# Performance work log

Measured on AMD Instinct MI355X. Metric: run time of the kernel, lower is better.

The kernel has to match this reference:

```python
import jax, jax.numpy as jnp
import numpy as np

B, D, H, E, K = 4096, 1024, 4096, 8, 2

def setup_inputs() -> dict:
    key = jax.random.key(0)
    ks = jax.random.split(key, 6)
    return {
        "x_modality": jax.random.normal(ks[0], (B, D), dtype=jnp.float32),
        "expert_indices": jax.random.randint(ks[1], (B, K), 0, E, dtype=jnp.int32),
        "hard_weights": jax.random.uniform(ks[2], (B, K), dtype=jnp.float32),
        "w1": jax.random.normal(ks[3], (E, D, H), dtype=jnp.float32) * (1.0 / np.sqrt(D)),
        "b1": jnp.zeros((E, H), dtype=jnp.float32),
        "w2": jax.random.normal(ks[4], (E, H, D), dtype=jnp.float32) * (1.0 / np.sqrt(H)),
        "b2": jnp.zeros((E, D), dtype=jnp.float32),
    }

def reference(x_modality, expert_indices, hard_weights, w1, b1, w2, b2):
    b = x_modality.shape[0]
    # Per-token gate per expert: sum of hard_weights over top_k slots routed to that expert.
    gates = jnp.zeros((b, E), dtype=x_modality.dtype)
    gates = gates.at[jnp.arange(b)[:, None], expert_indices].add(hard_weights)  # [b, E]
    # Dense expert compute (small fixed E), then gated combine.
    h = jax.nn.gelu(jnp.einsum("bd,edh->ebh", x_modality, w1) + b1[:, None, :], approximate=False)
    y = jnp.einsum("ebh,ehd->ebd", h, w2) + b2[:, None, :]  # [E, b, D]
    return jnp.einsum("be,ebd->bd", gates, y)
```

## Files before the change

kernel.cpp:

```cpp
#include <hip/hip_runtime.h>
#include <hip/hip_bf16.h>
#include <math.h>

#define NB 4096
#define ND 1024
#define NH 4096
#define NE 8
#define NKK 2
#define NROWS (NB*NKK)
#define MAXT 72

typedef __attribute__((ext_vector_type(8))) short short8;
typedef __attribute__((ext_vector_type(4))) float f32x4;

__device__ __forceinline__ void gload_lds16(const void* g, void* l) {
    __builtin_amdgcn_global_load_lds(
        (const __attribute__((address_space(1))) unsigned int*)g,
        (__attribute__((address_space(3))) unsigned int*)l, 16, 0, 0);
}

__device__ __forceinline__ unsigned short f2bf(float f) {
    __hip_bfloat16 h = __float2bfloat16(f);
    return *reinterpret_cast<unsigned short*>(&h);
}

__device__ __forceinline__ float fast_gelu(float x) {
    float xs  = x * 0.70710678118654752f;
    float axs = fabsf(xs);
    float t   = __builtin_amdgcn_rcpf(1.0f + 0.3275911f * axs);
    float p   = t * (0.254829592f + t * (-0.284496736f + t * (1.421413741f +
                t * (-1.453152027f + t * 1.061405429f))));
    float e   = __expf(-xs * xs);
    float erf_abs = 1.0f - p * e;
    float erf = copysignf(erf_abs, x);
    return 0.5f * x * (1.0f + erf);
}


__global__ void k_cvt_x(const float* __restrict__ in, __hip_bfloat16* __restrict__ out, int n8) {
    int i = blockIdx.x * 256 + threadIdx.x;
    if (i >= n8) return;
    const float4* p = reinterpret_cast<const float4*>(in) + (size_t)i * 2;
    float4 a = p[0], b = p[1];
    ushort4 lo, hi;
    lo.x = f2bf(a.x); lo.y = f2bf(a.y); lo.z = f2bf(a.z); lo.w = f2bf(a.w);
    hi.x = f2bf(b.x); hi.y = f2bf(b.y); hi.z = f2bf(b.z); hi.w = f2bf(b.w);
    reinterpret_cast<ushort4*>(out)[(size_t)i*2]   = lo;
    reinterpret_cast<ushort4*>(out)[(size_t)i*2+1] = hi;
}

__global__ void k_transpose_cvt(const float* __restrict__ in, __hip_bfloat16* __restrict__ out,
                                int R, int C) {
    __shared__ float tile[64][68];
    const size_t ebase = (size_t)blockIdx.z * R * C;
    const int r0 = blockIdx.y * 64, c0 = blockIdx.x * 64;
    const int t = threadIdx.x;
    const int lr = t >> 4, lc4 = (t & 15) * 4;
    #pragma unroll
    for (int i = 0; i < 4; ++i) {
        int r = lr + i * 16;
        float4 v = *reinterpret_cast<const float4*>(&in[ebase + (size_t)(r0 + r) * C + (c0 + lc4)]);
        *reinterpret_cast<float4*>(&tile[r][lc4]) = v;
    }
    __syncthreads();
    const int q = t & 15, cw = t >> 4;
    #pragma unroll
    for (int i = 0; i < 4; ++i) {
        int cc = cw + i * 16;
        ushort4 v;
        v.x = f2bf(tile[q*4+0][cc]);
        v.y = f2bf(tile[q*4+1][cc]);
        v.z = f2bf(tile[q*4+2][cc]);
        v.w = f2bf(tile[q*4+3][cc]);
        *reinterpret_cast<ushort4*>(&out[ebase + (size_t)(c0 + cc) * R + (r0 + q*4)]) = v;
    }
}


__global__ void k_route_count(const int* __restrict__ idx, int* cnt) {
    int b = blockIdx.x * 256 + threadIdx.x;
    if (b < NB) {
        atomicAdd(&cnt[idx[2*b]], 1);
        atomicAdd(&cnt[idx[2*b+1]], 1);
    }
}

__global__ void k_route_scan(const int* __restrict__ cnt, int* offs, int* cursor,
                             int* tile_e, int* tile_row, int* ntiles) {
    if (threadIdx.x == 0) {
        int s = 0, t = 0;
        for (int e = 0; e < NE; ++e) {
            offs[e] = s; cursor[e] = s;
            for (int r = 0; r < cnt[e]; r += 128) {
                tile_e[t] = e; tile_row[t] = s + r; ++t;
            }
            s += cnt[e];
        }
        offs[NE] = s;
        *ntiles = t;
    }
}

__global__ void k_route_fill(const int* __restrict__ idx, const float* __restrict__ hw,
                             int* cursor, int* tok, float* gw) {
    int b = blockIdx.x * 256 + threadIdx.x;
    if (b < NB) {
        #pragma unroll
        for (int k = 0; k < NKK; ++k) {
            int e = idx[2*b + k];
            int p = atomicAdd(&cursor[e], 1);
            tok[p] = b;
            gw[p]  = hw[2*b + k];
        }
    }
}


template<int STAGE>
__global__ __launch_bounds__(256, 4) void moe_gemm(
    const __hip_bfloat16* __restrict__ Asrc,
    const __hip_bfloat16* __restrict__ Bt,
    const float* __restrict__ bias,
    __hip_bfloat16* __restrict__ Hout,
    float* __restrict__ Out,
    const int* __restrict__ offs,
    const int* __restrict__ tok,
    const float* __restrict__ gw,
    const int* __restrict__ tile_e,
    const int* __restrict__ tile_row,
    const int* __restrict__ ntiles)
{
    constexpr int N = (STAGE == 1) ? NH : ND;
    constexpr int K = (STAGE == 1) ? ND : NH;
    constexpr int NT_N = N / 128;
    constexpr int NTL = NT_N / 8;
    constexpr int TOTAL = NT_N * MAXT;

    const int bid = blockIdx.x;
    const int xcd = bid & 7;
    const int c = bid >> 3;
    const int tb  = c / (NTL * 9);
    const int rr  = c % (NTL * 9);
    const int ntl = rr / 9;
    const int tin = rr % 9;
    const int tile = tb * 9 + tin;
    const int nt = xcd * NTL + ntl;
    if (tile >= *ntiles) return;

    const int e = tile_e[tile];
    const int rowbase = tile_row[tile];
    const int end = offs[e + 1];

    __shared__ __align__(16) __hip_bfloat16 sA[128 * 64];
    __shared__ __align__(16) __hip_bfloat16 sB[128 * 64];

    const int tid = threadIdx.x;
    const int w = tid >> 6;
    const int l = tid & 63;

    const int srow = tid >> 3;
    const int schunk = (tid & 7) ^ (srow & 7);
    const __hip_bfloat16* aptr[4];
    const __hip_bfloat16* bptr[4];
    #pragma unroll
    for (int i = 0; i < 4; ++i) {
        int r = srow + i * 32;
        int re = rowbase + r; if (re > end - 1) re = end - 1;
        if (STAGE == 1) aptr[i] = Asrc + (size_t)tok[re] * ND + schunk * 8;
        else            aptr[i] = Asrc + (size_t)re * NH + schunk * 8;
        bptr[i] = Bt + ((size_t)e * N + (nt * 128 + r)) * K + schunk * 8;
    }
    __hip_bfloat16 *adst[4], *bdst[4];
    #pragma unroll
    for (int i = 0; i < 4; ++i) {
        adst[i] = sA + (i * 256 + w * 64) * 8;
        bdst[i] = sB + (i * 256 + w * 64) * 8;
    }

    const int wm = (w >> 1) * 64;
    const int wn = (w & 1) * 64;
    const int l15 = l & 15, l4 = l >> 4;

    f32x4 acc[4][4];
    #pragma unroll
    for (int mi = 0; mi < 4; ++mi)
        #pragma unroll
        for (int ni = 0; ni < 4; ++ni) acc[mi][ni] = (f32x4){0.f, 0.f, 0.f, 0.f};

    int aoff[4][2], boff[4][2];
    #pragma unroll
    for (int mi = 0; mi < 4; ++mi) {
        int row = wm + mi * 16 + l15;
        #pragma unroll
        for (int ks = 0; ks < 2; ++ks)
            aoff[mi][ks] = row * 128 + (((ks * 4 + l4) ^ (row & 7)) * 16);
    }
    #pragma unroll
    for (int ni = 0; ni < 4; ++ni) {
        int row = wn + ni * 16 + l15;
        #pragma unroll
        for (int ks = 0; ks < 2; ++ks)
            boff[ni][ks] = row * 128 + (((ks * 4 + l4) ^ (row & 7)) * 16);
    }

    const char* sAb = (const char*)sA;
    const char* sBb = (const char*)sB;

    for (int kt = 0; kt < K / 64; ++kt) {
        #pragma unroll
        for (int i = 0; i < 4; ++i) {
            gload_lds16(aptr[i] + kt * 64, adst[i]);
            gload_lds16(bptr[i] + kt * 64, bdst[i]);
        }
        __syncthreads();
        short8 af[4][2], bfr[4][2];
        #pragma unroll
        for (int mi = 0; mi < 4; ++mi)
            #pragma unroll
            for (int ks = 0; ks < 2; ++ks)
                af[mi][ks] = *(const short8*)(sAb + aoff[mi][ks]);
        #pragma unroll
        for (int ni = 0; ni < 4; ++ni)
            #pragma unroll
            for (int ks = 0; ks < 2; ++ks)
                bfr[ni][ks] = *(const short8*)(sBb + boff[ni][ks]);
        #pragma unroll
        for (int mi = 0; mi < 4; ++mi)
            #pragma unroll
            for (int ni = 0; ni < 4; ++ni)
                #pragma unroll
                for (int ks = 0; ks < 2; ++ks)
                    acc[mi][ni] = __builtin_amdgcn_mfma_f32_16x16x32_bf16(
                        af[mi][ks], bfr[ni][ks], acc[mi][ni], 0, 0, 0);
        __syncthreads();
    }

    const int ncol0 = nt * 128 + wn;
    #pragma unroll
    for (int mi = 0; mi < 4; ++mi) {
        #pragma unroll
        for (int ni = 0; ni < 4; ++ni) {
            int gn = ncol0 + ni * 16 + l15;
            float bv = bias[e * N + gn];
            #pragma unroll
            for (int j = 0; j < 4; ++j) {
                int re = rowbase + wm + mi * 16 + l4 * 4 + j;
                if (re < end) {
                    float v = acc[mi][ni][j] + bv;
                    if (STAGE == 1) {
                        Hout[(size_t)re * NH + gn] = __float2bfloat16(fast_gelu(v));
                    } else {
                        atomicAdd(&Out[(size_t)tok[re] * ND + gn], gw[re] * v);
                    }
                }
            }
        }
    }
}


extern "C" void kernel_launch(void* const* d_in, const int* in_sizes, int n_in,
                              void* d_out, int out_size, void* d_ws, size_t ws_size,
                              hipStream_t stream) {
    const float* x   = (const float*)d_in[0];
    const int*   idx = (const int*)d_in[1];
    const float* hw  = (const float*)d_in[2];
    const float* w1  = (const float*)d_in[3];
    const float* b1  = (const float*)d_in[4];
    const float* w2  = (const float*)d_in[5];
    const float* b2  = (const float*)d_in[6];
    float* out = (float*)d_out;

    char* ws = (char*)d_ws;
    size_t off = 0;
    __hip_bfloat16* xb  = (__hip_bfloat16*)(ws + off); off += (size_t)NB * ND * 2;
    __hip_bfloat16* w1t = (__hip_bfloat16*)(ws + off); off += (size_t)NE * ND * NH * 2;
    __hip_bfloat16* w2t = (__hip_bfloat16*)(ws + off); off += (size_t)NE * NH * ND * 2;
    __hip_bfloat16* h   = (__hip_bfloat16*)(ws + off); off += (size_t)NROWS * NH * 2;
    int*   tok     = (int*)(ws + off);   off += NROWS * 4;
    float* gwb     = (float*)(ws + off); off += NROWS * 4;
    int*   cnt     = (int*)(ws + off);   off += 16 * 4;
    int*   offs    = (int*)(ws + off);   off += 16 * 4;
    int*   cursor  = (int*)(ws + off);   off += 16 * 4;
    int*   tile_e  = (int*)(ws + off);   off += MAXT * 4;
    int*   tile_row= (int*)(ws + off);   off += MAXT * 4;
    int*   ntiles  = (int*)(ws + off);   off += 16 * 4;
    (void)ws_size; (void)in_sizes; (void)n_in; (void)out_size;

    hipMemsetAsync(d_out, 0, (size_t)NB * ND * sizeof(float), stream);
    hipMemsetAsync(cnt, 0, 16 * 4, stream);

    k_cvt_x<<<dim3((NB * ND / 8 + 255) / 256), 256, 0, stream>>>(x, xb, NB * ND / 8);
    k_transpose_cvt<<<dim3(NH / 64, ND / 64, NE), 256, 0, stream>>>(w1, w1t, ND, NH);
    k_transpose_cvt<<<dim3(ND / 64, NH / 64, NE), 256, 0, stream>>>(w2, w2t, NH, ND);
    k_route_count<<<dim3((NB + 255) / 256), 256, 0, stream>>>(idx, cnt);
    k_route_scan<<<1, 64, 0, stream>>>(cnt, offs, cursor, tile_e, tile_row, ntiles);
    k_route_fill<<<dim3((NB + 255) / 256), 256, 0, stream>>>(idx, hw, cursor, tok, gwb);

    moe_gemm<1><<<dim3((NH / 128) * MAXT), 256, 0, stream>>>(
        xb, w1t, b1, h, nullptr, offs, tok, gwb, tile_e, tile_row, ntiles);
    moe_gemm<2><<<dim3((ND / 128) * MAXT), 256, 0, stream>>>(
        h, w2t, b2, nullptr, out, offs, tok, gwb, tile_e, tile_row, ntiles);
}
```

Measured before the change: 404.5 us.

## Enlarge MoE GEMM tiles to 256 rows, double-buffer LDS, split-K second stage

Routing tiles grow from 128 to 256 rows. Both grouped GEMMs now run with 512 threads, larger block tiles (256x256 in stage 1, 256x128 in stage 2) and double-buffered LDS staging through dynamic shared memory, with MFMA sections raised to higher wave priority. The x conversion becomes a gather into expert-sorted row order, so stage 1 reads A contiguously. Stage 2 splits K into two halves across XCD pairs, which doubles the atomic adds into the output. The aim is more data reuse per block and loads that overlap compute, at the cost of lower occupancy and more atomic traffic.

```diff
diff --git a/kernel.cpp b/kernel.cpp
--- a/kernel.cpp
+++ b/kernel.cpp
@@ -8,7 +8,7 @@
 #define NE 8
 #define NKK 2
 #define NROWS (NB*NKK)
-#define MAXT 72
+#define MAXT2 40
 
 typedef __attribute__((ext_vector_type(8))) short short8;
 typedef __attribute__((ext_vector_type(4))) float f32x4;
@@ -37,18 +37,6 @@
 }
 
 
-__global__ void k_cvt_x(const float* __restrict__ in, __hip_bfloat16* __restrict__ out, int n8) {
-    int i = blockIdx.x * 256 + threadIdx.x;
-    if (i >= n8) return;
-    const float4* p = reinterpret_cast<const float4*>(in) + (size_t)i * 2;
-    float4 a = p[0], b = p[1];
-    ushort4 lo, hi;
-    lo.x = f2bf(a.x); lo.y = f2bf(a.y); lo.z = f2bf(a.z); lo.w = f2bf(a.w);
-    hi.x = f2bf(b.x); hi.y = f2bf(b.y); hi.z = f2bf(b.z); hi.w = f2bf(b.w);
-    reinterpret_cast<ushort4*>(out)[(size_t)i*2]   = lo;
-    reinterpret_cast<ushort4*>(out)[(size_t)i*2+1] = hi;
-}
-
 __global__ void k_transpose_cvt(const float* __restrict__ in, __hip_bfloat16* __restrict__ out,
                                 int R, int C) {
     __shared__ float tile[64][68];
@@ -91,7 +79,7 @@
         int s = 0, t = 0;
         for (int e = 0; e < NE; ++e) {
             offs[e] = s; cursor[e] = s;
-            for (int r = 0; r < cnt[e]; r += 128) {
+            for (int r = 0; r < cnt[e]; r += 256) {
                 tile_e[t] = e; tile_row[t] = s + r; ++t;
             }
             s += cnt[e];
@@ -115,9 +103,17 @@
     }
 }
 
+__global__ void k_gather_cvt(const float* __restrict__ x, const int* __restrict__ tok,
+                             __hip_bfloat16* __restrict__ Ag) {
+    const int row = blockIdx.x;
+    const float4 v = reinterpret_cast<const float4*>(x + (size_t)tok[row] * ND)[threadIdx.x];
+    ushort4 u; u.x = f2bf(v.x); u.y = f2bf(v.y); u.z = f2bf(v.z); u.w = f2bf(v.w);
+    reinterpret_cast<ushort4*>(Ag + (size_t)row * ND)[threadIdx.x] = u;
+}
+
 
 template<int STAGE>
-__global__ __launch_bounds__(256, 4) void moe_gemm(
+__global__ __launch_bounds__(512, 2) void moe_gemm(
     const __hip_bfloat16* __restrict__ Asrc,
     const __hip_bfloat16* __restrict__ Bt,
     const float* __restrict__ bias,
@@ -130,126 +126,119 @@
     const int* __restrict__ tile_row,
     const int* __restrict__ ntiles)
 {
-    constexpr int N = (STAGE == 1) ? NH : ND;
-    constexpr int K = (STAGE == 1) ? ND : NH;
-    constexpr int NT_N = N / 128;
-    constexpr int NTL = NT_N / 8;
-    constexpr int TOTAL = NT_N * MAXT;
+    constexpr int N   = (STAGE == 1) ? NH : ND;
+    constexpr int K   = (STAGE == 1) ? ND : NH;
+    constexpr int BN  = (STAGE == 1) ? 256 : 128;
+    constexpr int KT  = (STAGE == 1) ? 16 : 32;
+    constexpr int NI  = BN / 64;
+    constexpr int BR  = (BN * 64) / (512 * 8);
+    constexpr int ASZ = 256 * 64;
+    constexpr int BUF = ASZ + BN * 64;
+
+    extern __shared__ __hip_bfloat16 smem[];
 
     const int bid = blockIdx.x;
     const int xcd = bid & 7;
-    const int c = bid >> 3;
-    const int tb  = c / (NTL * 9);
-    const int rr  = c % (NTL * 9);
-    const int ntl = rr / 9;
-    const int tin = rr % 9;
-    const int tile = tb * 9 + tin;
-    const int nt = xcd * NTL + ntl;
+    const int c   = bid >> 3;
+    const int tile = (xcd >> 1) * 10 + (c >> 3);
+    const int sub  = c & 7;
     if (tile >= *ntiles) return;
+
+    int nt, kbase;
+    if (STAGE == 1) { nt = (xcd & 1) * 8 + sub; kbase = 0; }
+    else            { nt = sub;                 kbase = (xcd & 1) * (NH / 2); }
 
     const int e = tile_e[tile];
     const int rowbase = tile_row[tile];
     const int end = offs[e + 1];
 
-    __shared__ __align__(16) __hip_bfloat16 sA[128 * 64];
-    __shared__ __align__(16) __hip_bfloat16 sB[128 * 64];
-
     const int tid = threadIdx.x;
-    const int w = tid >> 6;
-    const int l = tid & 63;
-
+    const int w = tid >> 6, l = tid & 63;
     const int srow = tid >> 3;
     const int schunk = (tid & 7) ^ (srow & 7);
+
     const __hip_bfloat16* aptr[4];
-    const __hip_bfloat16* bptr[4];
-    #pragma unroll
-    for (int i = 0; i < 4; ++i) {
-        int r = srow + i * 32;
-        int re = rowbase + r; if (re > end - 1) re = end - 1;
-        if (STAGE == 1) aptr[i] = Asrc + (size_t)tok[re] * ND + schunk * 8;
-        else            aptr[i] = Asrc + (size_t)re * NH + schunk * 8;
-        bptr[i] = Bt + ((size_t)e * N + (nt * 128 + r)) * K + schunk * 8;
-    }
-    __hip_bfloat16 *adst[4], *bdst[4];
-    #pragma unroll
-    for (int i = 0; i < 4; ++i) {
-        adst[i] = sA + (i * 256 + w * 64) * 8;
-        bdst[i] = sB + (i * 256 + w * 64) * 8;
-    }
-
-    const int wm = (w >> 1) * 64;
-    const int wn = (w & 1) * 64;
+    #pragma unroll
+    for (int r = 0; r < 4; ++r) {
+        int re = rowbase + srow + r * 64; if (re > end - 1) re = end - 1;
+        aptr[r] = Asrc + (size_t)re * K + kbase + schunk * 8;
+    }
+    const __hip_bfloat16* bptr[BR];
+    #pragma unroll
+    for (int r = 0; r < BR; ++r)
+        bptr[r] = Bt + ((size_t)e * N + (size_t)(nt * BN + srow + r * 64)) * K + kbase + schunk * 8;
+
+    const int wm  = (w >> 2) * 128;
+    const int wn  = (w & 3) * (BN / 4);
     const int l15 = l & 15, l4 = l >> 4;
 
-    f32x4 acc[4][4];
-    #pragma unroll
-    for (int mi = 0; mi < 4; ++mi)
-        #pragma unroll
-        for (int ni = 0; ni < 4; ++ni) acc[mi][ni] = (f32x4){0.f, 0.f, 0.f, 0.f};
-
-    int aoff[4][2], boff[4][2];
-    #pragma unroll
-    for (int mi = 0; mi < 4; ++mi) {
-        int row = wm + mi * 16 + l15;
-        #pragma unroll
-        for (int ks = 0; ks < 2; ++ks)
-            aoff[mi][ks] = row * 128 + (((ks * 4 + l4) ^ (row & 7)) * 16);
-    }
-    #pragma unroll
-    for (int ni = 0; ni < 4; ++ni) {
-        int row = wn + ni * 16 + l15;
-        #pragma unroll
-        for (int ks = 0; ks < 2; ++ks)
-            boff[ni][ks] = row * 128 + (((ks * 4 + l4) ^ (row & 7)) * 16);
-    }
-
-    const char* sAb = (const char*)sA;
-    const char* sBb = (const char*)sB;
-
-    for (int kt = 0; kt < K / 64; ++kt) {
-        #pragma unroll
-        for (int i = 0; i < 4; ++i) {
-            gload_lds16(aptr[i] + kt * 64, adst[i]);
-            gload_lds16(bptr[i] + kt * 64, bdst[i]);
-        }
+    const int cs[2] = { ((l4) ^ (l15 & 7)) * 16, ((4 + l4) ^ (l15 & 7)) * 16 };
+    const int abase = (wm + l15) * 128;
+    const int bbase = (wn + l15) * 128;
+
+    f32x4 acc[8][NI];
+    #pragma unroll
+    for (int mi = 0; mi < 8; ++mi)
+        #pragma unroll
+        for (int ni = 0; ni < NI; ++ni) acc[mi][ni] = (f32x4){0.f, 0.f, 0.f, 0.f};
+
+    auto stage_t = [&](int b, int kt) {
+        __hip_bfloat16* da = smem + b * BUF;
+        __hip_bfloat16* db = da + ASZ;
+        #pragma unroll
+        for (int r = 0; r < 4; ++r)  gload_lds16(aptr[r] + kt * 64, da + tid * 8 + r * 4096);
+        #pragma unroll
+        for (int r = 0; r < BR; ++r) gload_lds16(bptr[r] + kt * 64, db + tid * 8 + r * 4096);
+    };
+
+    stage_t(0, 0);
+    __syncthreads();
+
+    int cur = 0;
+    #pragma unroll 1
+    for (int kt = 0; kt < KT; ++kt) {
+        if (kt + 1 < KT) stage_t(cur ^ 1, kt + 1);
+        const char* sa = (const char*)(smem + cur * BUF);
+        const char* sb = (const char*)(smem + cur * BUF + ASZ);
+        __builtin_amdgcn_s_setprio(1);
+        #pragma unroll
+        for (int ks = 0; ks < 2; ++ks) {
+            short8 af[8], bfv[NI];
+            #pragma unroll
+            for (int mi = 0; mi < 8; ++mi)
+                af[mi] = *(const short8*)(sa + abase + mi * 2048 + cs[ks]);
+            #pragma unroll
+            for (int ni = 0; ni < NI; ++ni)
+                bfv[ni] = *(const short8*)(sb + bbase + ni * 2048 + cs[ks]);
+            #pragma unroll
+            for (int mi = 0; mi < 8; ++mi)
+                #pragma unroll
+                for (int ni = 0; ni < NI; ++ni)
+                    acc[mi][ni] = __builtin_amdgcn_mfma_f32_16x16x32_bf16(
+                        af[mi], bfv[ni], acc[mi][ni], 0, 0, 0);
+        }
+        __builtin_amdgcn_s_setprio(0);
         __syncthreads();
-        short8 af[4][2], bfr[4][2];
-        #pragma unroll
-        for (int mi = 0; mi < 4; ++mi)
-            #pragma unroll
-            for (int ks = 0; ks < 2; ++ks)
-                af[mi][ks] = *(const short8*)(sAb + aoff[mi][ks]);
-        #pragma unroll
-        for (int ni = 0; ni < 4; ++ni)
-            #pragma unroll
-            for (int ks = 0; ks < 2; ++ks)
-                bfr[ni][ks] = *(const short8*)(sBb + boff[ni][ks]);
-        #pragma unroll
-        for (int mi = 0; mi < 4; ++mi)
-            #pragma unroll
-            for (int ni = 0; ni < 4; ++ni)
-                #pragma unroll
-                for (int ks = 0; ks < 2; ++ks)
-                    acc[mi][ni] = __builtin_amdgcn_mfma_f32_16x16x32_bf16(
-                        af[mi][ks], bfr[ni][ks], acc[mi][ni], 0, 0, 0);
-        __syncthreads();
-    }
-
-    const int ncol0 = nt * 128 + wn;
-    #pragma unroll
-    for (int mi = 0; mi < 4; ++mi) {
-        #pragma unroll
-        for (int ni = 0; ni < 4; ++ni) {
-            int gn = ncol0 + ni * 16 + l15;
-            float bv = bias[e * N + gn];
+        cur ^= 1;
+    }
+
+    const int ncol0 = nt * BN + wn;
+    #pragma unroll
+    for (int mi = 0; mi < 8; ++mi) {
+        #pragma unroll
+        for (int ni = 0; ni < NI; ++ni) {
+            const int gn = ncol0 + ni * 16 + l15;
+            const float bv = bias[e * N + gn];
             #pragma unroll
             for (int j = 0; j < 4; ++j) {
-                int re = rowbase + wm + mi * 16 + l4 * 4 + j;
+                const int re = rowbase + wm + mi * 16 + l4 * 4 + j;
                 if (re < end) {
-                    float v = acc[mi][ni][j] + bv;
+                    float v = acc[mi][ni][j];
                     if (STAGE == 1) {
+                        v += bv;
                         Hout[(size_t)re * NH + gn] = __float2bfloat16(fast_gelu(v));
                     } else {
+                        if (kbase == 0) v += bv;
                         atomicAdd(&Out[(size_t)tok[re] * ND + gn], gw[re] * v);
                     }
                 }
@@ -273,7 +262,7 @@
 
     char* ws = (char*)d_ws;
     size_t off = 0;
-    __hip_bfloat16* xb  = (__hip_bfloat16*)(ws + off); off += (size_t)NB * ND * 2;
+    __hip_bfloat16* Ag  = (__hip_bfloat16*)(ws + off); off += (size_t)NROWS * ND * 2;
     __hip_bfloat16* w1t = (__hip_bfloat16*)(ws + off); off += (size_t)NE * ND * NH * 2;
     __hip_bfloat16* w2t = (__hip_bfloat16*)(ws + off); off += (size_t)NE * NH * ND * 2;
     __hip_bfloat16* h   = (__hip_bfloat16*)(ws + off); off += (size_t)NROWS * NH * 2;
@@ -282,23 +271,28 @@
     int*   cnt     = (int*)(ws + off);   off += 16 * 4;
     int*   offs    = (int*)(ws + off);   off += 16 * 4;
     int*   cursor  = (int*)(ws + off);   off += 16 * 4;
-    int*   tile_e  = (int*)(ws + off);   off += MAXT * 4;
-    int*   tile_row= (int*)(ws + off);   off += MAXT * 4;
+    int*   tile_e  = (int*)(ws + off);   off += MAXT2 * 4;
+    int*   tile_row= (int*)(ws + off);   off += MAXT2 * 4;
     int*   ntiles  = (int*)(ws + off);   off += 16 * 4;
     (void)ws_size; (void)in_sizes; (void)n_in; (void)out_size;
 
+    hipFuncSetAttribute((const void*)moe_gemm<1>,
+                        hipFuncAttributeMaxDynamicSharedMemorySize, 131072);
+    hipFuncSetAttribute((const void*)moe_gemm<2>,
+                        hipFuncAttributeMaxDynamicSharedMemorySize, 98304);
+
     hipMemsetAsync(d_out, 0, (size_t)NB * ND * sizeof(float), stream);
     hipMemsetAsync(cnt, 0, 16 * 4, stream);
 
-    k_cvt_x<<<dim3((NB * ND / 8 + 255) / 256), 256, 0, stream>>>(x, xb, NB * ND / 8);
-    k_transpose_cvt<<<dim3(NH / 64, ND / 64, NE), 256, 0, stream>>>(w1, w1t, ND, NH);
-    k_transpose_cvt<<<dim3(ND / 64, NH / 64, NE), 256, 0, stream>>>(w2, w2t, NH, ND);
     k_route_count<<<dim3((NB + 255) / 256), 256, 0, stream>>>(idx, cnt);
     k_route_scan<<<1, 64, 0, stream>>>(cnt, offs, cursor, tile_e, tile_row, ntiles);
     k_route_fill<<<dim3((NB + 255) / 256), 256, 0, stream>>>(idx, hw, cursor, tok, gwb);
-
-    moe_gemm<1><<<dim3((NH / 128) * MAXT), 256, 0, stream>>>(
-        xb, w1t, b1, h, nullptr, offs, tok, gwb, tile_e, tile_row, ntiles);
-    moe_gemm<2><<<dim3((ND / 128) * MAXT), 256, 0, stream>>>(
+    k_gather_cvt<<<dim3(NROWS), 256, 0, stream>>>(x, tok, Ag);
+    k_transpose_cvt<<<dim3(NH / 64, ND / 64, NE), 256, 0, stream>>>(w1, w1t, ND, NH);
+    k_transpose_cvt<<<dim3(ND / 64, NH / 64, NE), 256, 0, stream>>>(w2, w2t, NH, ND);
+
+    moe_gemm<1><<<dim3(16 * MAXT2), 512, 131072, stream>>>(
+        Ag, w1t, b1, h, nullptr, offs, tok, gwb, tile_e, tile_row, ntiles);
+    moe_gemm<2><<<dim3(16 * MAXT2), 512, 98304, stream>>>(
         h, w2t, b2, nullptr, out, offs, tok, gwb, tile_e, tile_row, ntiles);
 }
```

Result: slower. 492.8 us (+21.8%).

## Pre-gather routed token rows, remap tile schedule, split-K stage two GEMM

Applied to the files above, without the earlier changes.

Replaces the dense x conversion with a gather kernel that writes bf16 copies of the routed token rows contiguously, so stage one no longer loads A through a token index. The block-to-tile mapping is reworked so each XCD pair covers a group of tiles and N-tiles, and stage two splits K in half across XCDs, doubling its grid and relying on the existing atomic accumulation, with bias added only once. Weight transposes are moved to sit just before their GEMMs. The split-K doubles the number of atomics into the output, and the fixed remap assumes MAXT=72 tiles.

```diff
diff --git a/kernel.cpp b/kernel.cpp
--- a/kernel.cpp
+++ b/kernel.cpp
@@ -36,18 +36,6 @@
     return 0.5f * x * (1.0f + erf);
 }
 
-
-__global__ void k_cvt_x(const float* __restrict__ in, __hip_bfloat16* __restrict__ out, int n8) {
-    int i = blockIdx.x * 256 + threadIdx.x;
-    if (i >= n8) return;
-    const float4* p = reinterpret_cast<const float4*>(in) + (size_t)i * 2;
-    float4 a = p[0], b = p[1];
-    ushort4 lo, hi;
-    lo.x = f2bf(a.x); lo.y = f2bf(a.y); lo.z = f2bf(a.z); lo.w = f2bf(a.w);
-    hi.x = f2bf(b.x); hi.y = f2bf(b.y); hi.z = f2bf(b.z); hi.w = f2bf(b.w);
-    reinterpret_cast<ushort4*>(out)[(size_t)i*2]   = lo;
-    reinterpret_cast<ushort4*>(out)[(size_t)i*2+1] = hi;
-}
 
 __global__ void k_transpose_cvt(const float* __restrict__ in, __hip_bfloat16* __restrict__ out,
                                 int R, int C) {
@@ -113,6 +101,14 @@
             gw[p]  = hw[2*b + k];
         }
     }
+}
+
+__global__ void k_gather_cvt(const float* __restrict__ x, const int* __restrict__ tok,
+                             __hip_bfloat16* __restrict__ Ag) {
+    const int row = blockIdx.x;
+    const float4 v = reinterpret_cast<const float4*>(x + (size_t)tok[row] * ND)[threadIdx.x];
+    ushort4 u; u.x = f2bf(v.x); u.y = f2bf(v.y); u.z = f2bf(v.z); u.w = f2bf(v.w);
+    reinterpret_cast<ushort4*>(Ag + (size_t)row * ND)[threadIdx.x] = u;
 }
 
 
@@ -130,21 +126,24 @@
     const int* __restrict__ tile_row,
     const int* __restrict__ ntiles)
 {
-    constexpr int N = (STAGE == 1) ? NH : ND;
-    constexpr int K = (STAGE == 1) ? ND : NH;
-    constexpr int NT_N = N / 128;
-    constexpr int NTL = NT_N / 8;
-    constexpr int TOTAL = NT_N * MAXT;
+    constexpr int N    = (STAGE == 1) ? NH : ND;
+    constexpr int KROW = (STAGE == 1) ? ND : NH;
+    constexpr int KT   = (STAGE == 1) ? 16 : 32;
 
     const int bid = blockIdx.x;
     const int xcd = bid & 7;
-    const int c = bid >> 3;
-    const int tb  = c / (NTL * 9);
-    const int rr  = c % (NTL * 9);
-    const int ntl = rr / 9;
-    const int tin = rr % 9;
-    const int tile = tb * 9 + tin;
-    const int nt = xcd * NTL + ntl;
+    const int c   = bid >> 3;
+    int tile, nt, kbase;
+    if (STAGE == 1) {
+        const int cell = c / 72, rr = c % 72;
+        tile = (xcd >> 1) * 18 + (cell & 1) * 9 + rr % 9;
+        nt   = (xcd & 1) * 16 + (cell >> 1) * 8 + rr / 9;
+        kbase = 0;
+    } else {
+        tile = (xcd >> 1) * 18 + (c / 72) * 9 + (c % 72) % 9;
+        nt   = (c % 72) / 9;
+        kbase = (xcd & 1) * (NH / 2);
+    }
     if (tile >= *ntiles) return;
 
     const int e = tile_e[tile];
@@ -166,9 +165,8 @@
     for (int i = 0; i < 4; ++i) {
         int r = srow + i * 32;
         int re = rowbase + r; if (re > end - 1) re = end - 1;
-        if (STAGE == 1) aptr[i] = Asrc + (size_t)tok[re] * ND + schunk * 8;
-        else            aptr[i] = Asrc + (size_t)re * NH + schunk * 8;
-        bptr[i] = Bt + ((size_t)e * N + (nt * 128 + r)) * K + schunk * 8;
+        aptr[i] = Asrc + (size_t)re * KROW + kbase + schunk * 8;
+        bptr[i] = Bt + ((size_t)e * N + (nt * 128 + r)) * KROW + kbase + schunk * 8;
     }
     __hip_bfloat16 *adst[4], *bdst[4];
     #pragma unroll
@@ -206,7 +204,7 @@
     const char* sAb = (const char*)sA;
     const char* sBb = (const char*)sB;
 
-    for (int kt = 0; kt < K / 64; ++kt) {
+    for (int kt = 0; kt < KT; ++kt) {
         #pragma unroll
         for (int i = 0; i < 4; ++i) {
             gload_lds16(aptr[i] + kt * 64, adst[i]);
@@ -246,10 +244,12 @@
             for (int j = 0; j < 4; ++j) {
                 int re = rowbase + wm + mi * 16 + l4 * 4 + j;
                 if (re < end) {
-                    float v = acc[mi][ni][j] + bv;
+                    float v = acc[mi][ni][j];
                     if (STAGE == 1) {
+                        v += bv;
                         Hout[(size_t)re * NH + gn] = __float2bfloat16(fast_gelu(v));
                     } else {
+                        if (kbase == 0) v += bv;
                         atomicAdd(&Out[(size_t)tok[re] * ND + gn], gw[re] * v);
                     }
                 }
@@ -273,7 +273,7 @@
 
     char* ws = (char*)d_ws;
     size_t off = 0;
-    __hip_bfloat16* xb  = (__hip_bfloat16*)(ws + off); off += (size_t)NB * ND * 2;
+    __hip_bfloat16* Ag  = (__hip_bfloat16*)(ws + off); off += (size_t)NROWS * ND * 2;
     __hip_bfloat16* w1t = (__hip_bfloat16*)(ws + off); off += (size_t)NE * ND * NH * 2;
     __hip_bfloat16* w2t = (__hip_bfloat16*)(ws + off); off += (size_t)NE * NH * ND * 2;
     __hip_bfloat16* h   = (__hip_bfloat16*)(ws + off); off += (size_t)NROWS * NH * 2;
@@ -290,15 +290,16 @@
     hipMemsetAsync(d_out, 0, (size_t)NB * ND * sizeof(float), stream);
     hipMemsetAsync(cnt, 0, 16 * 4, stream);
 
-    k_cvt_x<<<dim3((NB * ND / 8 + 255) / 256), 256, 0, stream>>>(x, xb, NB * ND / 8);
-    k_transpose_cvt<<<dim3(NH / 64, ND / 64, NE), 256, 0, stream>>>(w1, w1t, ND, NH);
-    k_transpose_cvt<<<dim3(ND / 64, NH / 64, NE), 256, 0, stream>>>(w2, w2t, NH, ND);
     k_route_count<<<dim3((NB + 255) / 256), 256, 0, stream>>>(idx, cnt);
     k_route_scan<<<1, 64, 0, stream>>>(cnt, offs, cursor, tile_e, tile_row, ntiles);
     k_route_fill<<<dim3((NB + 255) / 256), 256, 0, stream>>>(idx, hw, cursor, tok, gwb);
-
-    moe_gemm<1><<<dim3((NH / 128) * MAXT), 256, 0, stream>>>(
-        xb, w1t, b1, h, nullptr, offs, tok, gwb, tile_e, tile_row, ntiles);
-    moe_gemm<2><<<dim3((ND / 128) * MAXT), 256, 0, stream>>>(
+    k_gather_cvt<<<dim3(NROWS), 256, 0, stream>>>(x, tok, Ag);
+
+    k_transpose_cvt<<<dim3(NH / 64, ND / 64, NE), 256, 0, stream>>>(w1, w1t, ND, NH);
+    moe_gemm<1><<<dim3(8 * 288), 256, 0, stream>>>(
+        Ag, w1t, b1, h, nullptr, offs, tok, gwb, tile_e, tile_row, ntiles);
+
+    k_transpose_cvt<<<dim3(ND / 64, NH / 64, NE), 256, 0, stream>>>(w2, w2t, NH, ND);
+    moe_gemm<2><<<dim3(8 * 144), 256, 0, stream>>>(
         h, w2t, b2, nullptr, out, offs, tok, gwb, tile_e, tile_row, ntiles);
 }
```

Measured after the change: 427.6 us. 5.7% more time.
